# Kernel optimization log

Measured on AMD Instinct MI355X. Metric: run time of the kernel, lower is better.

Reference implementation:

```python
import jax, jax.numpy as jnp
import numpy as np

W_BITS = 4
IN_FEATURES = 4096
OUT_FEATURES = 4096
# clamp bounds used by the module: finfo(fp16).max * (1 - 0.005)
FP16_MAX = float(np.finfo(np.float16).max) * (1.0 - 0.005)


def _dequant(qweight, lut, w_bits):
    """Bitplane LUT dequant.

    qweight: (w_bits, O, I//32) int32 bitplanes; bit j%32 of word j//32 on
    plane p holds bit (w_bits-1-p) of weight code [o, j] (MSB-first planes).
    lut: (O, 2**w_bits) per-output-channel lookup table.
    Returns dense weight (O, I).
    """
    nb, O, G = qweight.shape
    shifts = jnp.arange(32, dtype=jnp.int32)
    # (w_bits, O, G, 32) -> (w_bits, O, I)
    bits = ((qweight[..., None] >> shifts) & 1).reshape(w_bits, O, G * 32)
    place = (jnp.int32(1) << jnp.arange(w_bits - 1, -1, -1, dtype=jnp.int32))
    codes = jnp.sum(bits * place[:, None, None], axis=0)  # (O, I) in [0, 2**w_bits)
    return jnp.take_along_axis(lut, codes, axis=1)  # (O, I)


def setup_inputs() -> dict:
    key = jax.random.key(0)
    k_x, k_q, k_l, k_b = jax.random.split(key, 4)
    x = jax.random.normal(k_x, (8, 2048, IN_FEATURES), dtype=jnp.float16)
    qweight = jax.random.randint(
        k_q, (W_BITS, OUT_FEATURES, IN_FEATURES // 32),
        minval=-(2**31), maxval=2**31 - 1, dtype=jnp.int32)
    lut = jax.random.normal(k_l, (OUT_FEATURES, 2**W_BITS), dtype=jnp.float16) * jnp.float16(0.05)
    bias = jax.random.normal(k_b, (OUT_FEATURES,), dtype=jnp.float16) * jnp.float16(0.05)
    return {"x": x, "qweight": qweight, "lut": lut, "bias": bias}


def reference(x, qweight, lut, bias):
    # Batched path of AnyPrecisionLinear.forward: dequant full weight, x @ W.T
    weight = _dequant(qweight, lut, W_BITS).astype(x.dtype)  # (O, I)
    y = jnp.einsum('bsi,oi->bso', x, weight)
    y = y + bias
    return jnp.clip(y, -FP16_MAX, FP16_MAX)
```

## Files before the change

### kernel.cpp

```cpp
#include <hip/hip_runtime.h>
#include <hip/hip_fp16.h>


using f16x8 = __attribute__((ext_vector_type(8))) _Float16;
using f32x4 = __attribute__((ext_vector_type(4))) float;

#define IN_F   4096
#define OUT_F  4096
#define M_ROWS 16384
#define PLANE_STRIDE (OUT_F * (IN_F / 32))
#define CLAMP_V 65176.484375f

union h8 {
  _Float16 h[8];
  uint4 v;
};

__global__ __launch_bounds__(256) void dequant_kernel(
    const int* __restrict__ qw, const float* __restrict__ lut,
    _Float16* __restrict__ W) {
  __shared__ _Float16 luts[32];
  const int t = threadIdx.x;
  if (t < 32) luts[t] = (_Float16)lut[blockIdx.x * 32 + t];
  __syncthreads();

  const int o = (blockIdx.x << 1) + (t >> 7);
  const int g = t & 127;
  const int base = o * (IN_F / 32) + g;

  const unsigned w0 = (unsigned)qw[base];
  const unsigned w1 = (unsigned)qw[base + PLANE_STRIDE];
  const unsigned w2 = (unsigned)qw[base + 2 * PLANE_STRIDE];
  const unsigned w3 = (unsigned)qw[base + 3 * PLANE_STRIDE];
  const int lo = (t >> 7) << 4;

  h8 out[4];
#pragma unroll
  for (int b = 0; b < 32; ++b) {
    unsigned code = (((w0 >> b) & 1u) << 3) | (((w1 >> b) & 1u) << 2) |
                    (((w2 >> b) & 1u) << 1) | ((w3 >> b) & 1u);
    out[b >> 3].h[b & 7] = luts[lo + code];
  }

  uint4* dst = (uint4*)&W[(size_t)o * IN_F + g * 32];
#pragma unroll
  for (int i = 0; i < 4; ++i) dst[i] = out[i].v;
}

__device__ __forceinline__ void tile_indices(int bid, int& mt, int& nt) {
  const int swz = (bid & 7) * 512 + (bid >> 3);
  mt = swz & 127;
  nt = swz >> 7;
}

__global__ __launch_bounds__(256) void gemm_ws(
    const float* __restrict__ X, const _Float16* __restrict__ W,
    const float* __restrict__ bias, float* __restrict__ Y) {
  __shared__ _Float16 As[128 * 32];
  __shared__ _Float16 Bs[128 * 32];

  const int t = threadIdx.x;
  const int lane = t & 63;
  const int wv = t >> 6;
  const int wm = wv >> 1;
  const int wn = wv & 1;

  int mt, nt;
  tile_indices(blockIdx.x, mt, nt);

  const int srow = t >> 1;
  const int hb = (t & 1) * 16;
  const size_t ax = (size_t)(mt * 128 + srow) * IN_F + hb;
  const size_t bx = (size_t)(nt * 128 + srow) * IN_F + hb;

  f32x4 acc[4][4] = {};
  const int frow = lane & 15;
  const int koff = (lane >> 4) * 8;

  for (int kt = 0; kt < IN_F / 32; ++kt) {
    const int k0 = kt * 32;
    h8 a0, a1;
#pragma unroll
    for (int c = 0; c < 2; ++c) {
      const float4 v0 = *(const float4*)&X[ax + k0 + c * 8];
      const float4 v1 = *(const float4*)&X[ax + k0 + c * 8 + 4];
      a0.h[c * 4 + 0] = (_Float16)v0.x; a0.h[c * 4 + 1] = (_Float16)v0.y;
      a0.h[c * 4 + 2] = (_Float16)v0.z; a0.h[c * 4 + 3] = (_Float16)v0.w;
      (void)v1;
      a1.h[c * 4 + 0] = (_Float16)v1.x; a1.h[c * 4 + 1] = (_Float16)v1.y;
      a1.h[c * 4 + 2] = (_Float16)v1.z; a1.h[c * 4 + 3] = (_Float16)v1.w;
    }
    h8 w0, w1;
    w0.h[0] = a0.h[0]; w0.h[1] = a0.h[1]; w0.h[2] = a0.h[2]; w0.h[3] = a0.h[3];
    w0.h[4] = a1.h[0]; w0.h[5] = a1.h[1]; w0.h[6] = a1.h[2]; w0.h[7] = a1.h[3];
    w1.h[0] = a0.h[4]; w1.h[1] = a0.h[5]; w1.h[2] = a0.h[6]; w1.h[3] = a0.h[7];
    w1.h[4] = a1.h[4]; w1.h[5] = a1.h[5]; w1.h[6] = a1.h[6]; w1.h[7] = a1.h[7];
    *(uint4*)&As[srow * 32 + hb] = w0.v;
    *(uint4*)&As[srow * 32 + hb + 8] = w1.v;
    *(uint4*)&Bs[srow * 32 + hb] = *(const uint4*)&W[bx + k0];
    *(uint4*)&Bs[srow * 32 + hb + 8] = *(const uint4*)&W[bx + k0 + 8];
    __syncthreads();

    f16x8 af[4], bf[4];
#pragma unroll
    for (int i = 0; i < 4; ++i) {
      af[i] = *(const f16x8*)&As[(wm * 64 + i * 16 + frow) * 32 + koff];
      bf[i] = *(const f16x8*)&Bs[(wn * 64 + i * 16 + frow) * 32 + koff];
    }
#pragma unroll
    for (int i = 0; i < 4; ++i)
#pragma unroll
      for (int j = 0; j < 4; ++j)
        acc[i][j] = __builtin_amdgcn_mfma_f32_16x16x32_f16(af[i], bf[j],
                                                           acc[i][j], 0, 0, 0);
    __syncthreads();
  }

  const int col_base = nt * 128 + wn * 64 + (lane & 15);
  const int row_base = mt * 128 + wm * 64 + (lane >> 4) * 4;
#pragma unroll
  for (int j = 0; j < 4; ++j) {
    const int col = col_base + j * 16;
    const float bv = bias[col];
#pragma unroll
    for (int i = 0; i < 4; ++i) {
      const int row = row_base + i * 16;
#pragma unroll
      for (int r = 0; r < 4; ++r) {
        float v = acc[i][j][r] + bv;
        v = fminf(fmaxf(v, -CLAMP_V), CLAMP_V);
        Y[(size_t)(row + r) * OUT_F + col] = v;
      }
    }
  }
}

__global__ __launch_bounds__(256) void gemm_fused(
    const float* __restrict__ X, const int* __restrict__ qw,
    const float* __restrict__ lut, const float* __restrict__ bias,
    float* __restrict__ Y) {
  __shared__ _Float16 As[128 * 32];
  __shared__ _Float16 Bs[128 * 32];
  __shared__ _Float16 lutS[128 * 16];

  const int t = threadIdx.x;
  const int lane = t & 63;
  const int wv = t >> 6;
  const int wm = wv >> 1;
  const int wn = wv & 1;

  int mt, nt;
  tile_indices(blockIdx.x, mt, nt);

  {
    h8 lv;
#pragma unroll
    for (int c = 0; c < 8; ++c)
      lv.h[c] = (_Float16)lut[(size_t)(nt * 128) * 16 + t * 8 + c];
    *(uint4*)&lutS[t * 8] = lv.v;
  }

  const int srow = t >> 1;
  const int hb = (t & 1) * 16;
  const size_t ax = (size_t)(mt * 128 + srow) * IN_F + hb;
  const int qb = (nt * 128 + srow) * (IN_F / 32);

  f32x4 acc[4][4] = {};
  const int frow = lane & 15;
  const int koff = (lane >> 4) * 8;

  __syncthreads();

  for (int kt = 0; kt < IN_F / 32; ++kt) {
    const int k0 = kt * 32;
    h8 w0, w1;
    {
      const float4 v0 = *(const float4*)&X[ax + k0];
      const float4 v1 = *(const float4*)&X[ax + k0 + 4];
      const float4 v2 = *(const float4*)&X[ax + k0 + 8];
      const float4 v3 = *(const float4*)&X[ax + k0 + 12];
      w0.h[0] = (_Float16)v0.x; w0.h[1] = (_Float16)v0.y;
      w0.h[2] = (_Float16)v0.z; w0.h[3] = (_Float16)v0.w;
      w0.h[4] = (_Float16)v1.x; w0.h[5] = (_Float16)v1.y;
      w0.h[6] = (_Float16)v1.z; w0.h[7] = (_Float16)v1.w;
      w1.h[0] = (_Float16)v2.x; w1.h[1] = (_Float16)v2.y;
      w1.h[2] = (_Float16)v2.z; w1.h[3] = (_Float16)v2.w;
      w1.h[4] = (_Float16)v3.x; w1.h[5] = (_Float16)v3.y;
      w1.h[6] = (_Float16)v3.z; w1.h[7] = (_Float16)v3.w;
    }
    *(uint4*)&As[srow * 32 + hb] = w0.v;
    *(uint4*)&As[srow * 32 + hb + 8] = w1.v;
    {
      const int base = qb + kt;
      const unsigned q0 = (unsigned)qw[base];
      const unsigned q1 = (unsigned)qw[base + PLANE_STRIDE];
      const unsigned q2 = (unsigned)qw[base + 2 * PLANE_STRIDE];
      const unsigned q3 = (unsigned)qw[base + 3 * PLANE_STRIDE];
      const _Float16* lr = &lutS[srow * 16];
      h8 t0, t1;
#pragma unroll
      for (int b2 = 0; b2 < 16; ++b2) {
        const int b = hb + b2;
        unsigned code = (((q0 >> b) & 1u) << 3) | (((q1 >> b) & 1u) << 2) |
                        (((q2 >> b) & 1u) << 1) | ((q3 >> b) & 1u);
        if (b2 < 8) t0.h[b2] = lr[code];
        else t1.h[b2 - 8] = lr[code];
      }
      *(uint4*)&Bs[srow * 32 + hb] = t0.v;
      *(uint4*)&Bs[srow * 32 + hb + 8] = t1.v;
    }
    __syncthreads();

    f16x8 af[4], bf[4];
#pragma unroll
    for (int i = 0; i < 4; ++i) {
      af[i] = *(const f16x8*)&As[(wm * 64 + i * 16 + frow) * 32 + koff];
      bf[i] = *(const f16x8*)&Bs[(wn * 64 + i * 16 + frow) * 32 + koff];
    }
#pragma unroll
    for (int i = 0; i < 4; ++i)
#pragma unroll
      for (int j = 0; j < 4; ++j)
        acc[i][j] = __builtin_amdgcn_mfma_f32_16x16x32_f16(af[i], bf[j],
                                                           acc[i][j], 0, 0, 0);
    __syncthreads();
  }

  const int col_base = nt * 128 + wn * 64 + (lane & 15);
  const int row_base = mt * 128 + wm * 64 + (lane >> 4) * 4;
#pragma unroll
  for (int j = 0; j < 4; ++j) {
    const int col = col_base + j * 16;
    const float bv = bias[col];
#pragma unroll
    for (int i = 0; i < 4; ++i) {
      const int row = row_base + i * 16;
#pragma unroll
      for (int r = 0; r < 4; ++r) {
        float v = acc[i][j][r] + bv;
        v = fminf(fmaxf(v, -CLAMP_V), CLAMP_V);
        Y[(size_t)(row + r) * OUT_F + col] = v;
      }
    }
  }
}

extern "C" void kernel_launch(void* const* d_in, const int* in_sizes, int n_in,
                              void* d_out, int out_size, void* d_ws,
                              size_t ws_size, hipStream_t stream) {
  const float* X = (const float*)d_in[0];
  const int* qw = (const int*)d_in[1];
  const float* lut = (const float*)d_in[2];
  const float* bias = (const float*)d_in[3];
  float* Y = (float*)d_out;

  const size_t w_bytes = (size_t)OUT_F * IN_F * sizeof(_Float16);
  const int grid = (M_ROWS / 128) * (OUT_F / 128);

  if (ws_size >= w_bytes && d_ws != nullptr) {
    _Float16* W16 = (_Float16*)d_ws;
    dequant_kernel<<<OUT_F / 2, 256, 0, stream>>>(qw, lut, W16);
    gemm_ws<<<grid, 256, 0, stream>>>(X, W16, bias, Y);
  } else {
    gemm_fused<<<grid, 256, 0, stream>>>(X, qw, lut, bias, Y);
  }
}
```

Baseline: 1.663 ms.

## Load weight tile via global_load_lds, swap tile raster order, simplify A staging

The GEMM now loads the B (weight) tile straight from global memory into LDS with the async global_load_lds builtin, so those values no longer pass through registers. The block-to-tile mapping is swapped so consecutive blocks walk the N dimension instead of M, which changes which X and W tiles share L2. The X staging code is rewritten into a simpler, contiguous conversion. The correctness of the LDS layout depends on how global_load_lds places each lane's 16 bytes relative to the per-wave base pointer, and the loop has no explicit wait on the async load before the barrier.

```diff
diff --git a/kernel.cpp b/kernel.cpp
--- a/kernel.cpp
+++ b/kernel.cpp
@@ -47,10 +47,16 @@
   for (int i = 0; i < 4; ++i) dst[i] = out[i].v;
 }
 
+__device__ __forceinline__ void gl_lds16(const void* g, void* l) {
+  __builtin_amdgcn_global_load_lds(
+      (const __attribute__((address_space(1))) void*)g,
+      (__attribute__((address_space(3))) void*)l, 16, 0, 0);
+}
+
 __device__ __forceinline__ void tile_indices(int bid, int& mt, int& nt) {
   const int swz = (bid & 7) * 512 + (bid >> 3);
-  mt = swz & 127;
-  nt = swz >> 7;
+  nt = swz & 31;
+  mt = swz >> 5;
 }
 
 __global__ __launch_bounds__(256) void gemm_ws(
@@ -71,7 +77,12 @@
   const int srow = t >> 1;
   const int hb = (t & 1) * 16;
   const size_t ax = (size_t)(mt * 128 + srow) * IN_F + hb;
-  const size_t bx = (size_t)(nt * 128 + srow) * IN_F + hb;
+
+  const int r0 = t >> 2;
+  const int q0 = (t & 3) * 8;
+  const size_t b_off0 = (size_t)(nt * 128 + r0) * IN_F + q0;
+  const size_t b_off1 = (size_t)(nt * 128 + r0 + 64) * IN_F + q0;
+  _Float16* Bs_d = &Bs[wv * 512];
 
   f32x4 acc[4][4] = {};
   const int frow = lane & 15;
@@ -79,26 +90,25 @@
 
   for (int kt = 0; kt < IN_F / 32; ++kt) {
     const int k0 = kt * 32;
-    h8 a0, a1;
-#pragma unroll
-    for (int c = 0; c < 2; ++c) {
-      const float4 v0 = *(const float4*)&X[ax + k0 + c * 8];
-      const float4 v1 = *(const float4*)&X[ax + k0 + c * 8 + 4];
-      a0.h[c * 4 + 0] = (_Float16)v0.x; a0.h[c * 4 + 1] = (_Float16)v0.y;
-      a0.h[c * 4 + 2] = (_Float16)v0.z; a0.h[c * 4 + 3] = (_Float16)v0.w;
-      (void)v1;
-      a1.h[c * 4 + 0] = (_Float16)v1.x; a1.h[c * 4 + 1] = (_Float16)v1.y;
-      a1.h[c * 4 + 2] = (_Float16)v1.z; a1.h[c * 4 + 3] = (_Float16)v1.w;
-    }
+    gl_lds16(&W[b_off0 + k0], Bs_d);
+    gl_lds16(&W[b_off1 + k0], Bs_d + 2048);
     h8 w0, w1;
-    w0.h[0] = a0.h[0]; w0.h[1] = a0.h[1]; w0.h[2] = a0.h[2]; w0.h[3] = a0.h[3];
-    w0.h[4] = a1.h[0]; w0.h[5] = a1.h[1]; w0.h[6] = a1.h[2]; w0.h[7] = a1.h[3];
-    w1.h[0] = a0.h[4]; w1.h[1] = a0.h[5]; w1.h[2] = a0.h[6]; w1.h[3] = a0.h[7];
-    w1.h[4] = a1.h[4]; w1.h[5] = a1.h[5]; w1.h[6] = a1.h[6]; w1.h[7] = a1.h[7];
+    {
+      const float4 v0 = *(const float4*)&X[ax + k0];
+      const float4 v1 = *(const float4*)&X[ax + k0 + 4];
+      const float4 v2 = *(const float4*)&X[ax + k0 + 8];
+      const float4 v3 = *(const float4*)&X[ax + k0 + 12];
+      w0.h[0] = (_Float16)v0.x; w0.h[1] = (_Float16)v0.y;
+      w0.h[2] = (_Float16)v0.z; w0.h[3] = (_Float16)v0.w;
+      w0.h[4] = (_Float16)v1.x; w0.h[5] = (_Float16)v1.y;
+      w0.h[6] = (_Float16)v1.z; w0.h[7] = (_Float16)v1.w;
+      w1.h[0] = (_Float16)v2.x; w1.h[1] = (_Float16)v2.y;
+      w1.h[2] = (_Float16)v2.z; w1.h[3] = (_Float16)v2.w;
+      w1.h[4] = (_Float16)v3.x; w1.h[5] = (_Float16)v3.y;
+      w1.h[6] = (_Float16)v3.z; w1.h[7] = (_Float16)v3.w;
+    }
     *(uint4*)&As[srow * 32 + hb] = w0.v;
     *(uint4*)&As[srow * 32 + hb + 8] = w1.v;
-    *(uint4*)&Bs[srow * 32 + hb] = *(const uint4*)&W[bx + k0];
-    *(uint4*)&Bs[srow * 32 + hb + 8] = *(const uint4*)&W[bx + k0 + 8];
     __syncthreads();
 
     f16x8 af[4], bf[4];
```

Result: faster. 1.364 ms (-18.0%).
